# Performance work log

Hardware: AMD Instinct MI355X
Metric: run time of the kernel (lower is better)

Reference implementation:

```python
import jax, jax.numpy as jnp
import numpy as np

B, H, W, C, NH = 16, 56, 56, 192, 6
N = H * W
HD = C // NH
EPS = 1e-5


def _ln(x, g, b):
    m = jnp.mean(x, -1, keepdims=True)
    v = jnp.mean((x - m) ** 2, -1, keepdims=True)
    return (x - m) * jax.lax.rsqrt(v + EPS) * g + b


def _dwconv(x, w, b):
    # x: (B,H,W,Ch), w: (3,3,1,Ch) depthwise, SAME padding
    y = jax.lax.conv_general_dilated(
        x, w, (1, 1), 'SAME',
        dimension_numbers=('NHWC', 'HWIO', 'NHWC'),
        feature_group_count=x.shape[-1])
    return y + b


def _rope_tables():
    k_max = C // 4  # 2D RoPE: feature_dim // (2 * num_spatial_dims)
    theta = 1.0 / (10000.0 ** (jnp.arange(k_max, dtype=jnp.float32) / k_max))
    ai = jnp.arange(H, dtype=jnp.float32)[:, None, None] * theta
    aj = jnp.arange(W, dtype=jnp.float32)[None, :, None] * theta
    ang = jnp.concatenate([jnp.broadcast_to(ai, (H, W, k_max)),
                           jnp.broadcast_to(aj, (H, W, k_max))], -1)  # (H,W,C//2)
    return jnp.cos(ang), jnp.sin(ang)


def _rope(x, cos, sin):
    # x: (B,H,W,C); complex multiply on interleaved (re,im) pairs
    xr, xi = x[..., 0::2], x[..., 1::2]
    return jnp.stack([cos * xr - sin * xi, cos * xi + sin * xr], -1).reshape(x.shape)


def reference(x, cpe1_w, cpe1_b, norm1_g, norm1_b, in_w, in_b, actp_w, actp_b,
              dwc_w, dwc_b, qk_w, qk_b, lepe_w, lepe_b, outp_w, outp_b,
              cpe2_w, cpe2_b, norm2_g, norm2_b, fc1_w, fc1_b, mdw_w, mdw_b,
              fc2_w, fc2_b, mn1_g, mn1_b, mn2_g, mn2_b, mn3_g, mn3_b):
    img = lambda t: t.reshape(B, H, W, -1)
    seq = lambda t: t.reshape(B, N, -1)

    # CPE1
    x = x + seq(_dwconv(img(x), cpe1_w, cpe1_b))
    shortcut = x
    xn = _ln(x, norm1_g, norm1_b)

    # gated branch
    act_res = jax.nn.silu(xn @ actp_w + actp_b)
    h = seq(jax.nn.silu(_dwconv(img(xn @ in_w + in_b), dwc_w, dwc_b)))

    # --- LinearAttention (ELU+1 kernel, RoPE, LePE) ---
    qk = h @ qk_w + qk_b                      # (B,N,2C)
    q = jax.nn.elu(qk[..., :C]) + 1.0
    k = jax.nn.elu(qk[..., C:]) + 1.0
    cos, sin = _rope_tables()
    q_r = seq(_rope(img(q), cos, sin)).reshape(B, N, NH, HD)
    k_r = seq(_rope(img(k), cos, sin)).reshape(B, N, NH, HD)
    q4 = q.reshape(B, N, NH, HD)
    k4 = k.reshape(B, N, NH, HD)
    v4 = h.reshape(B, N, NH, HD)
    kmean = jnp.mean(k4, axis=1)                                  # (B,NH,HD)
    z = 1.0 / (jnp.einsum('bnhd,bhd->bnh', q4, kmean) + 1e-6)     # (B,N,NH)
    kv = jnp.einsum('bnhd,bnhe->bhde', k_r, v4) / N               # (B,NH,HD,HD)
    attn = jnp.einsum('bnhd,bhde->bnhe', q_r, kv) * z[..., None]
    attn = attn.reshape(B, N, C)
    attn = attn + seq(_dwconv(img(h), lepe_w, lepe_b))            # LePE on v

    x = shortcut + (attn * act_res) @ outp_w + outp_b

    # CPE2
    x = x + seq(_dwconv(img(x), cpe2_w, cpe2_b))

    # FRN MLP: fc1 -> dwconv -> 3 chained residual LayerNorms -> GELU -> fc2
    xm = _ln(x, norm2_g, norm2_b)
    f1 = xm @ fc1_w + fc1_b                   # (B,N,768)
    dw = seq(_dwconv(img(f1), mdw_w, mdw_b))
    n1 = _ln(dw + f1, mn1_g, mn1_b)
    n2 = _ln(n1 + f1, mn2_g, mn2_b)
    n3 = _ln(n2 + f1, mn3_g, mn3_b)
    x = x + jax.nn.gelu(n3, approximate=False) @ fc2_w + fc2_b
    return x


def setup_inputs() -> dict:
    key = jax.random.key(0)
    cnt = [0]
    def rn(shape, s=0.05):
        cnt[0] += 1
        return jax.random.normal(jax.random.fold_in(key, cnt[0]), shape, jnp.float32) * s
    dws = (3, 3, 1, C)
    z = lambda n: jnp.zeros((n,), jnp.float32)
    o = lambda n: jnp.ones((n,), jnp.float32)
    return dict(
        x=rn((B, N, C), 1.0),
        cpe1_w=rn(dws), cpe1_b=z(C),
        norm1_g=o(C), norm1_b=z(C),
        in_w=rn((C, C)), in_b=z(C),
        actp_w=rn((C, C)), actp_b=z(C),
        dwc_w=rn(dws), dwc_b=z(C),
        qk_w=rn((C, 2 * C)), qk_b=z(2 * C),
        lepe_w=rn(dws), lepe_b=z(C),
        outp_w=rn((C, C)), outp_b=z(C),
        cpe2_w=rn(dws), cpe2_b=z(C),
        norm2_g=o(C), norm2_b=z(C),
        fc1_w=rn((C, 4 * C)), fc1_b=z(4 * C),
        mdw_w=rn((3, 3, 1, 4 * C)), mdw_b=z(4 * C),
        fc2_w=rn((4 * C, C)), fc2_b=z(C),
        mn1_g=o(4 * C), mn1_b=z(4 * C),
        mn2_g=o(4 * C), mn2_b=z(4 * C),
        mn3_g=o(4 * C), mn3_b=z(4 * C),
    )
```

## Files before the change

kernel.cpp:

```cpp
#include <hip/hip_runtime.h>
#include <hip/hip_bf16.h>
#include <hip/hip_fp16.h>
#include <math.h>

#define BB 16
#define HH 56
#define WW 56
#define CC0 192
#define NHH 6
#define HDD 32
#define NPOS (HH*WW)
#define MROWS (BB*NPOS)
#define C4 (4*CC0)

typedef __hip_bfloat16 bf16;
typedef __half f16;
typedef short short8 __attribute__((ext_vector_type(8)));
typedef short short4v __attribute__((ext_vector_type(4)));
typedef float f32x4 __attribute__((ext_vector_type(4)));
typedef float f32x2 __attribute__((ext_vector_type(2)));
typedef unsigned int u32;
typedef u32 u32x4 __attribute__((ext_vector_type(4)));
typedef u32 u32x2 __attribute__((ext_vector_type(2)));

__device__ __forceinline__ float b2f(bf16 v){ return __bfloat162float(v); }
__device__ __forceinline__ bf16 f2b(float v){ return __float2bfloat16(v); }
__device__ __forceinline__ short f2s(float v){ bf16 b = __float2bfloat16(v); return *(short*)&b; }
__device__ __forceinline__ float s2f(short s){ bf16 b; *(short*)&b = s; return __bfloat162float(b); }
__device__ __forceinline__ float tof(float v){ return v; }
__device__ __forceinline__ float tof(f16 v){ return __half2float(v); }
__device__ __forceinline__ f32x2 bfp(u32 u){
  union { u32 q; float f; } lo, hi;
  lo.q = u << 16; hi.q = u & 0xffff0000u;
  return (f32x2){lo.f, hi.f};
}
__device__ __forceinline__ float fast_gelu(float x){
  float u = 1.5957691216f * (x + 0.044715f*x*x*x);
  float t = 1.f - 2.f/(__expf(u) + 1.f);
  return 0.5f*x*(1.f + t);
}
__device__ __forceinline__ int swz8(int bid, int nblk){
  return (bid & 7) * (nblk >> 3) + (bid >> 3);
}

__global__ __launch_bounds__(256) void convert_weights(
    const float* __restrict__ w0, const float* __restrict__ w1,
    const float* __restrict__ w2, const float* __restrict__ w3,
    const float* __restrict__ w4, const float* __restrict__ w5,
    short* __restrict__ dst){
  int t = blockIdx.x*256 + threadIdx.x;
  int e = t*4;
  if (e >= 479232) return;
  const float* src; int K, N, off;
  if      (e <  36864){ src=w0; K=192; N=192; off=0; }
  else if (e <  73728){ src=w1; K=192; N=192; off=36864; }
  else if (e < 147456){ src=w2; K=192; N=384; off=73728; }
  else if (e < 184320){ src=w3; K=192; N=192; off=147456; }
  else if (e < 331776){ src=w4; K=192; N=768; off=184320; }
  else                { src=w5; K=768; N=192; off=331776; }
  int le = e - off;
  int n = le / K, k = le % K;
  short4v o;
  #pragma unroll
  for (int l = 0; l < 4; ++l) o[l] = f2s(src[(size_t)(k+l)*N + n]);
  *(short4v*)(dst + e) = o;
}

template<typename TIN>
__global__ __launch_bounds__(256) void cpe_ln_kernel(const TIN* __restrict__ in,
    const float* __restrict__ w, const float* __restrict__ bias,
    const float* __restrict__ g, const float* __restrict__ bb,
    f16* __restrict__ x1out, bf16* __restrict__ xnout){
  int wv = threadIdx.x >> 6, lane = threadIdx.x & 63;
  int grp = swz8(blockIdx.x, gridDim.x)*4 + wv;
  int pos0 = grp * 4;
  int b = pos0 / NPOS; int ij = pos0 % NPOS; int i = ij / WW; int j0 = ij % WW;
  int c = lane * 3;
  float acc[4][3];
  {
    float b0 = bias[c], b1 = bias[c+1], b2 = bias[c+2];
    #pragma unroll
    for (int p = 0; p < 4; ++p){ acc[p][0]=b0; acc[p][1]=b1; acc[p][2]=b2; }
  }
  float fc[4][3];
  bool leftOK  = (j0 > 0);
  bool rightOK = (j0 + 4 < WW);
  int base_i = (b*NPOS + i*WW + j0)*CC0 + c;

  #pragma unroll
  for (int di = 0; di < 3; ++di){
    int ii = i + di - 1;
    if (ii < 0 || ii >= HH) continue;
    int rb = base_i + (di-1)*(WW*CC0);
    float wt[3][3];
    #pragma unroll
    for (int dj = 0; dj < 3; ++dj){
      const float* wp = w + (di*3 + dj)*CC0 + c;
      wt[dj][0] = wp[0]; wt[dj][1] = wp[1]; wt[dj][2] = wp[2];
    }
    if (leftOK){
      const TIN* ip = in + rb - CC0;
      float d0 = tof(ip[0]), d1 = tof(ip[1]), d2 = tof(ip[2]);
      acc[0][0] += d0*wt[0][0]; acc[0][1] += d1*wt[0][1]; acc[0][2] += d2*wt[0][2];
    }
    #pragma unroll
    for (int col = 1; col <= 4; ++col){
      const TIN* ip = in + rb + (col-1)*CC0;
      float d0 = tof(ip[0]), d1 = tof(ip[1]), d2 = tof(ip[2]);
      if (di == 1){ fc[col-1][0] = d0; fc[col-1][1] = d1; fc[col-1][2] = d2; }
      #pragma unroll
      for (int dj = 0; dj < 3; ++dj){
        int p = col - dj;
        if (p >= 0 && p < 4){
          acc[p][0] += d0*wt[dj][0]; acc[p][1] += d1*wt[dj][1]; acc[p][2] += d2*wt[dj][2];
        }
      }
    }
    if (rightOK){
      const TIN* ip = in + rb + 4*CC0;
      float d0 = tof(ip[0]), d1 = tof(ip[1]), d2 = tof(ip[2]);
      acc[3][0] += d0*wt[2][0]; acc[3][1] += d1*wt[2][1]; acc[3][2] += d2*wt[2][2];
    }
  }
  float gv0 = g[c], gv1 = g[c+1], gv2 = g[c+2];
  float bv0 = bb[c], bv1 = bb[c+1], bv2 = bb[c+2];
  #pragma unroll
  for (int p = 0; p < 4; ++p){
    float v0 = fc[p][0] + acc[p][0];
    float v1 = fc[p][1] + acc[p][1];
    float v2 = fc[p][2] + acc[p][2];
    int base = (pos0 + p)*CC0 + c;
    f16* xp = x1out + base;
    xp[0] = __float2half(v0); xp[1] = __float2half(v1); xp[2] = __float2half(v2);
    float s = v0+v1+v2, q = v0*v0+v1*v1+v2*v2;
    #pragma unroll
    for (int m = 1; m < 64; m <<= 1){ s += __shfl_xor(s, m, 64); q += __shfl_xor(q, m, 64); }
    float mean = s * (1.f/CC0);
    float rstd = rsqrtf(q * (1.f/CC0) - mean*mean + 1e-5f);
    bf16* op = xnout + base;
    op[0] = f2b((v0-mean)*rstd*gv0 + bv0);
    op[1] = f2b((v1-mean)*rstd*gv1 + bv1);
    op[2] = f2b((v2-mean)*rstd*gv2 + bv2);
  }
}

template<int MODE>
__global__ __launch_bounds__(256) void dwconv4(const bf16* __restrict__ in,
    const float* __restrict__ w, const float* __restrict__ bias, void* __restrict__ out){
  int idx = swz8(blockIdx.x, gridDim.x)*256 + threadIdx.x;
  int cg = idx % 24; int quad = idx / 24;
  int pos0 = quad * 4;
  int b = pos0 / NPOS; int ij = pos0 % NPOS; int i = ij / WW; int j0 = ij % WW;
  int cb = cg * 8;
  const short* fp = (const short*)in;
  f32x2 acc[4][4];
  {
    f32x2 bv0 = *(const f32x2*)(bias + cb);
    f32x2 bv1 = *(const f32x2*)(bias + cb + 2);
    f32x2 bv2 = *(const f32x2*)(bias + cb + 4);
    f32x2 bv3 = *(const f32x2*)(bias + cb + 6);
    #pragma unroll
    for (int p = 0; p < 4; ++p){ acc[p][0]=bv0; acc[p][1]=bv1; acc[p][2]=bv2; acc[p][3]=bv3; }
  }
  bool leftOK  = (j0 > 0);
  bool rightOK = (j0 + 4 < WW);
  int base_i = (b*NPOS + i*WW + j0)*CC0 + cb;

  #pragma unroll
  for (int di = 0; di < 3; ++di){
    int ii = i + di - 1;
    if (ii < 0 || ii >= HH) continue;
    int rb = base_i + (di-1)*(WW*CC0);
    const float* wr = w + (di*3)*CC0 + cb;
    f32x2 wt[3][4];
    #pragma unroll
    for (int dj = 0; dj < 3; ++dj){
      #pragma unroll
      for (int l = 0; l < 4; ++l) wt[dj][l] = *(const f32x2*)(wr + dj*CC0 + 2*l);
    }
    if (leftOK){
      u32x4 x = *(const u32x4*)(fp + rb - CC0);
      #pragma unroll
      for (int l = 0; l < 4; ++l) acc[0][l] += bfp(x[l])*wt[0][l];
    }
    #pragma unroll
    for (int col = 1; col <= 4; ++col){
      u32x4 x = *(const u32x4*)(fp + rb + (col-1)*CC0);
      f32x2 dv[4];
      #pragma unroll
      for (int l = 0; l < 4; ++l) dv[l] = bfp(x[l]);
      #pragma unroll
      for (int dj = 0; dj < 3; ++dj){
        int p = col - dj;
        if (p >= 0 && p < 4){
          #pragma unroll
          for (int l = 0; l < 4; ++l) acc[p][l] += dv[l]*wt[dj][l];
        }
      }
    }
    if (rightOK){
      u32x4 x = *(const u32x4*)(fp + rb + 4*CC0);
      #pragma unroll
      for (int l = 0; l < 4; ++l) acc[3][l] += bfp(x[l])*wt[2][l];
    }
  }
  #pragma unroll
  for (int p = 0; p < 4; ++p){
    int oidx = (pos0 + p)*CC0 + cb;
    short8 o;
    if constexpr (MODE == 1){
      #pragma unroll
      for (int l = 0; l < 4; ++l){
        float a0 = acc[p][l][0], a1 = acc[p][l][1];
        o[2*l]   = f2s(a0/(1.f + expf(-a0)));
        o[2*l+1] = f2s(a1/(1.f + expf(-a1)));
      }
    } else {
      u32x4 r = *(const u32x4*)((const short*)out + oidx);
      #pragma unroll
      for (int l = 0; l < 4; ++l){
        f32x2 s = bfp(r[l]) + acc[p][l];
        o[2*l] = f2s(s[0]); o[2*l+1] = f2s(s[1]);
      }
    }
    *(short8*)((short*)out + oidx) = o;
  }
}

#define BM 256
#define BN 64
#define BK 32
#define LDA 40
template<int K, int N, int ALOAD, int EPI>
__global__ __launch_bounds__(256) void mfma_gemm(
    const void* __restrict__ a0v, const void* __restrict__ a1v,
    const short* __restrict__ wT, const float* __restrict__ bias,
    const void* __restrict__ addf, void* __restrict__ out0, void* __restrict__ out1){
  __shared__ short As[BM*LDA];
  __shared__ short Bs[BN*LDA];
  int tid = threadIdx.x;
  int wave = tid >> 6, lane = tid & 63;
  size_t m0 = (size_t)blockIdx.x * BM;
  int n0 = blockIdx.y * BN;
  int wm = wave * 64;
  int am = lane & 15, ak = (lane >> 4) * 8;

  f32x4 acc[4][4];
  #pragma unroll
  for (int mt = 0; mt < 4; ++mt)
    #pragma unroll
    for (int nt = 0; nt < 4; ++nt)
      acc[mt][nt] = (f32x4){0.f,0.f,0.f,0.f};

  for (int k0 = 0; k0 < K; k0 += BK){
    if constexpr (ALOAD == 0){
      const short* A = (const short*)a0v;
      #pragma unroll
      for (int it = 0; it < 4; ++it){
        int idx = it*256 + tid;
        int row = idx >> 2; int ko = (idx & 3) * 8;
        short8 v = *(const short8*)(A + (m0 + row)*(size_t)K + k0 + ko);
        *(short8*)&As[row*LDA + ko] = v;
      }
    } else {
      const short* A0p = (const short*)a0v;
      const short* A1p = (const short*)a1v;
      #pragma unroll
      for (int it = 0; it < 4; ++it){
        int idx = it*256 + tid;
        int row = idx >> 2; int ko = (idx & 3) * 8;
        size_t off = (m0 + row)*(size_t)K + k0 + ko;
        short8 va = *(const short8*)(A0p + off);
        short8 vb = *(const short8*)(A1p + off);
        short8 o;
        #pragma unroll
        for (int l = 0; l < 8; ++l) o[l] = f2s(s2f(va[l]) * s2f(vb[l]));
        *(short8*)&As[row*LDA + ko] = o;
      }
    }
    {
      int row = tid >> 2; int ko = (tid & 3) * 8;
      short8 v = *(const short8*)(wT + (size_t)(n0 + row)*K + k0 + ko);
      *(short8*)&Bs[row*LDA + ko] = v;
    }
    __syncthreads();
    short8 af[4], bfr[4];
    #pragma unroll
    for (int mt = 0; mt < 4; ++mt) af[mt] = *(short8*)&As[(wm + mt*16 + am)*LDA + ak];
    #pragma unroll
    for (int nt = 0; nt < 4; ++nt) bfr[nt] = *(short8*)&Bs[(nt*16 + am)*LDA + ak];
    #pragma unroll
    for (int mt = 0; mt < 4; ++mt)
      #pragma unroll
      for (int nt = 0; nt < 4; ++nt)
        acc[mt][nt] = __builtin_amdgcn_mfma_f32_16x16x32_bf16(af[mt], bfr[nt], acc[mt][nt], 0, 0, 0);
    __syncthreads();
  }

  int cn = lane & 15;
  int cr = (lane >> 4) * 4;
  #pragma unroll
  for (int mt = 0; mt < 4; ++mt){
    #pragma unroll
    for (int nt = 0; nt < 4; ++nt){
      int gn = n0 + nt*16 + cn;
      float bv;
      if constexpr (EPI == 4) bv = (n0 < CC0) ? bias[gn] : ((const float*)addf)[gn - CC0];
      else bv = bias[gn];
      #pragma unroll
      for (int r = 0; r < 4; ++r){
        size_t gm = m0 + wm + mt*16 + cr + r;
        float v = acc[mt][nt][r] + bv;
        if constexpr (EPI == 0){
          ((bf16*)out0)[gm*N + gn] = f2b(v);
        } else if constexpr (EPI == 1){
          ((bf16*)out0)[gm*N + gn] = f2b(v / (1.f + expf(-v)));
        } else if constexpr (EPI == 2){
          float rv = (v > 0.f) ? (v + 1.f) : expf(v);
          if (n0 < CC0) ((bf16*)out0)[gm*CC0 + gn] = f2b(rv);
          else          ((bf16*)out1)[gm*CC0 + (gn - CC0)] = f2b(rv);
        } else if constexpr (EPI == 4){
          if (n0 < CC0) ((bf16*)out0)[gm*CC0 + gn] = f2b(v / (1.f + expf(-v)));
          else          ((bf16*)out1)[gm*CC0 + (gn - CC0)] = f2b(v);
        } else if constexpr (EPI == 5){
          ((f16*)out0)[gm*N + gn] =
            __float2half(__half2float(((const f16*)addf)[gm*N + gn]) + v);
        } else {
          ((float*)out0)[gm*N + gn] =
            __half2float(((const f16*)addf)[gm*N + gn]) + v;
        }
      }
    }
  }
}

__global__ void rope_tables_kernel(float* __restrict__ cosT, float* __restrict__ sinT){
  int idx = blockIdx.x*256 + threadIdx.x;
  if (idx >= NPOS*96) return;
  int t = idx % 96; int ij = idx / 96; int i = ij / WW; int j = ij % WW;
  int kk = (t < 48) ? t : (t - 48);
  float th = expf(-(float)kk * 0.19188209108283716f);
  float pos = (t < 48) ? (float)i : (float)j;
  float ang = pos * th;
  cosT[idx] = cosf(ang);
  sinT[idx] = sinf(ang);
}

#define KVCH 14
__global__ __launch_bounds__(256) void kv_kernel(const bf16* __restrict__ kbuf,
    const bf16* __restrict__ hbuf, const float* __restrict__ cosT,
    const float* __restrict__ sinT, float* __restrict__ kv,
    float* __restrict__ kmean){
  int bi = blockIdx.x;
  int chunk = bi % KVCH; bi /= KVCH;
  int h = bi % NHH; int b = bi / NHH;
  int tid = threadIdx.x;
  int r8 = tid >> 5, lane = tid & 31;
  __shared__ float krs[8][32];
  __shared__ float vvs[8][32];
  int d = tid >> 3; int ebase = (tid & 7) * 4;
  float a0 = 0.f, a1 = 0.f, a2 = 0.f, a3 = 0.f;
  float ksum = 0.f;
  int c = h*HDD + lane;
  int t = c >> 1;
  bool odd = (lane & 1);
  for (int step = 0; step < NPOS/(KVCH*8); ++step){
    int n = chunk*(NPOS/KVCH) + step*8 + r8;
    size_t row = (size_t)b*NPOS + n;
    float kc = b2f(kbuf[row*CC0 + c]);
    float kp = b2f(kbuf[row*CC0 + (c ^ 1)]);
    ksum += kc;
    float cs = cosT[(size_t)n*96 + t], sn = sinT[(size_t)n*96 + t];
    krs[r8][lane] = odd ? (cs*kc + sn*kp) : (cs*kc - sn*kp);
    vvs[r8][lane] = b2f(hbuf[row*CC0 + c]);
    __syncthreads();
    #pragma unroll
    for (int nn = 0; nn < 8; ++nn){
      float kk2 = krs[nn][d];
      a0 += kk2 * vvs[nn][ebase+0];
      a1 += kk2 * vvs[nn][ebase+1];
      a2 += kk2 * vvs[nn][ebase+2];
      a3 += kk2 * vvs[nn][ebase+3];
    }
    __syncthreads();
  }
  const float invN = 1.f/NPOS;
  ksum += __shfl_xor(ksum, 32, 64);
  if ((tid & 32) == 0) atomicAdd(&kmean[b*CC0 + c], ksum * invN);
  float* kvp = kv + (((size_t)(b*NHH + h)*HDD + d)*HDD) + ebase;
  atomicAdd(kvp+0, a0*invN);
  atomicAdd(kvp+1, a1*invN);
  atomicAdd(kvp+2, a2*invN);
  atomicAdd(kvp+3, a3*invN);
}

__global__ __launch_bounds__(256) void attn_mfma(const bf16* __restrict__ q,
    const float* __restrict__ kmean, const float* __restrict__ kv,
    const float* __restrict__ cosT, const float* __restrict__ sinT,
    bf16* __restrict__ out){
  int w = threadIdx.x >> 6, lane = threadIdx.x & 63;
  int idx = blockIdx.x*4 + w;
  int mt = idx % (NPOS/16);
  int rest = idx / (NPOS/16);
  int h = rest % NHH; int b = rest / NHH;
  int r15 = lane & 15, kq = (lane >> 4) * 8;
  int n = mt*16 + r15;
  size_t row = (size_t)b*NPOS + n;
  int ch = h*HDD + kq;
  short8 q8 = *(const short8*)((const short*)q + row*CC0 + ch);
  float qf[8];
  #pragma unroll
  for (int j = 0; j < 8; ++j) qf[j] = s2f(q8[j]);
  const float* kmp = kmean + b*CC0 + ch;
  f32x4 km0 = *(const f32x4*)(kmp);
  f32x4 km1 = *(const f32x4*)(kmp + 4);
  float pm = qf[0]*km0[0]+qf[1]*km0[1]+qf[2]*km0[2]+qf[3]*km0[3]
           + qf[4]*km1[0]+qf[5]*km1[1]+qf[6]*km1[2]+qf[7]*km1[3];
  pm += __shfl_xor(pm, 16, 64);
  pm += __shfl_xor(pm, 32, 64);
  float z = 1.f/(pm + 1e-6f);
  int t0 = h*16 + (kq >> 1);
  f32x4 cs = *(const f32x4*)(cosT + n*96 + t0);
  f32x4 sn = *(const f32x4*)(sinT + n*96 + t0);
  short8 af;
  #pragma unroll
  for (int u = 0; u < 4; ++u){
    float e = cs[u]*qf[2*u]   - sn[u]*qf[2*u+1];
    float o = cs[u]*qf[2*u+1] + sn[u]*qf[2*u];
    af[2*u] = f2s(e); af[2*u+1] = f2s(o);
  }
  const float* kvp = kv + (size_t)(b*NHH + h)*HDD*HDD + kq*HDD + r15;
  short8 bf0, bf1;
  #pragma unroll
  for (int j = 0; j < 8; ++j){
    bf0[j] = f2s(kvp[j*HDD]);
    bf1[j] = f2s(kvp[j*HDD + 16]);
  }
  f32x4 acc0 = (f32x4){0.f,0.f,0.f,0.f};
  f32x4 acc1 = (f32x4){0.f,0.f,0.f,0.f};
  acc0 = __builtin_amdgcn_mfma_f32_16x16x32_bf16(af, bf0, acc0, 0, 0, 0);
  acc1 = __builtin_amdgcn_mfma_f32_16x16x32_bf16(af, bf1, acc1, 0, 0, 0);
  int rbase = (lane >> 4) * 4;
  #pragma unroll
  for (int r = 0; r < 4; ++r){
    float zz = __shfl(z, rbase + r, 64);
    size_t orow = (size_t)b*NPOS + mt*16 + rbase + r;
    out[orow*CC0 + ch - kq + r15]      = f2b(acc0[r]*zz);
    out[orow*CC0 + ch - kq + r15 + 16] = f2b(acc1[r]*zz);
  }
}

__global__ __launch_bounds__(256) void mdw_ln_kernel(const bf16* __restrict__ f1,
    const float* __restrict__ w, const float* __restrict__ bias,
    const float* __restrict__ g1, const float* __restrict__ b1,
    const float* __restrict__ g2, const float* __restrict__ b2,
    const float* __restrict__ g3, const float* __restrict__ b3,
    bf16* __restrict__ out){
  int wv = threadIdx.x >> 6, lane = threadIdx.x & 63;
  int grp = swz8(blockIdx.x, gridDim.x)*4 + wv;
  int pos0 = grp * 4;
  int b = pos0 / NPOS; int ij = pos0 % NPOS; int i = ij / WW; int j0 = ij % WW;
  int c0 = lane * 8;
  int c1 = 512 + lane * 4;
  const short* fp = (const short*)f1;

  f32x2 acc2[4][6];
  {
    f32x2 bv[6];
    #pragma unroll
    for (int l = 0; l < 4; ++l) bv[l] = *(const f32x2*)(bias + c0 + 2*l);
    bv[4] = *(const f32x2*)(bias + c1);
    bv[5] = *(const f32x2*)(bias + c1 + 2);
    #pragma unroll
    for (int p = 0; p < 4; ++p)
      #pragma unroll
      for (int l = 0; l < 6; ++l) acc2[p][l] = bv[l];
  }
  u32x4 fca[4]; u32x2 fcb[4];
  bool leftOK  = (j0 > 0);
  bool rightOK = (j0 + 4 < WW);
  int base_i = (b*NPOS + i*WW + j0)*C4;

  #pragma unroll
  for (int di = 0; di < 3; ++di){
    int ii = i + di - 1;
    if (ii < 0 || ii >= HH) continue;
    int rb = base_i + (di-1)*(WW*C4);
    f32x2 wt2[3][6];
    #pragma unroll
    for (int dj = 0; dj < 3; ++dj){
      const float* wp = w + (di*3 + dj)*C4;
      #pragma unroll
      for (int l = 0; l < 4; ++l) wt2[dj][l] = *(const f32x2*)(wp + c0 + 2*l);
      wt2[dj][4] = *(const f32x2*)(wp + c1);
      wt2[dj][5] = *(const f32x2*)(wp + c1 + 2);
    }
    if (leftOK){
      u32x4 xa = *(const u32x4*)(fp + rb - C4 + c0);
      u32x2 xb = *(const u32x2*)(fp + rb - C4 + c1);
      f32x2 dv[6];
      dv[0]=bfp(xa[0]); dv[1]=bfp(xa[1]); dv[2]=bfp(xa[2]); dv[3]=bfp(xa[3]);
      dv[4]=bfp(xb[0]); dv[5]=bfp(xb[1]);
      #pragma unroll
      for (int l = 0; l < 6; ++l) acc2[0][l] += dv[l]*wt2[0][l];
    }
    #pragma unroll
    for (int col = 1; col <= 4; ++col){
      int off = rb + (col-1)*C4;
      u32x4 xa = *(const u32x4*)(fp + off + c0);
      u32x2 xb = *(const u32x2*)(fp + off + c1);
      if (di == 1){ fca[col-1] = xa; fcb[col-1] = xb; }
      f32x2 dv[6];
      dv[0]=bfp(xa[0]); dv[1]=bfp(xa[1]); dv[2]=bfp(xa[2]); dv[3]=bfp(xa[3]);
      dv[4]=bfp(xb[0]); dv[5]=bfp(xb[1]);
      #pragma unroll
      for (int dj = 0; dj < 3; ++dj){
        int p = col - dj;
        if (p >= 0 && p < 4){
          #pragma unroll
          for (int l = 0; l < 6; ++l) acc2[p][l] += dv[l]*wt2[dj][l];
        }
      }
    }
    if (rightOK){
      u32x4 xa = *(const u32x4*)(fp + rb + 4*C4 + c0);
      u32x2 xb = *(const u32x2*)(fp + rb + 4*C4 + c1);
      f32x2 dv[6];
      dv[0]=bfp(xa[0]); dv[1]=bfp(xa[1]); dv[2]=bfp(xa[2]); dv[3]=bfp(xa[3]);
      dv[4]=bfp(xb[0]); dv[5]=bfp(xb[1]);
      #pragma unroll
      for (int l = 0; l < 6; ++l) acc2[3][l] += dv[l]*wt2[2][l];
    }
  }
  #pragma unroll
  for (int p = 0; p < 4; ++p){
    #pragma unroll
    for (int l = 0; l < 4; ++l) acc2[p][l] += bfp(fca[p][l]);
    acc2[p][4] += bfp(fcb[p][0]);
    acc2[p][5] += bfp(fcb[p][1]);
  }

  const float* gs[3] = {g1, g2, g3};
  const float* bs[3] = {b1, b2, b3};
  #pragma unroll
  for (int pass = 0; pass < 3; ++pass){
    f32x2 gv[6], bvv[6];
    #pragma unroll
    for (int l = 0; l < 4; ++l){
      gv[l]  = *(const f32x2*)(gs[pass] + c0 + 2*l);
      bvv[l] = *(const f32x2*)(bs[pass] + c0 + 2*l);
    }
    gv[4]  = *(const f32x2*)(gs[pass] + c1);  gv[5]  = *(const f32x2*)(gs[pass] + c1 + 2);
    bvv[4] = *(const f32x2*)(bs[pass] + c1);  bvv[5] = *(const f32x2*)(bs[pass] + c1 + 2);
    #pragma unroll
    for (int p = 0; p < 4; ++p){
      f32x2 s2 = acc2[p][0];
      f32x2 q2 = acc2[p][0]*acc2[p][0];
      #pragma unroll
      for (int l = 1; l < 6; ++l){ s2 += acc2[p][l]; q2 += acc2[p][l]*acc2[p][l]; }
      float s = s2[0]+s2[1], q = q2[0]+q2[1];
      #pragma unroll
      for (int m = 1; m < 64; m <<= 1){ s += __shfl_xor(s, m, 64); q += __shfl_xor(q, m, 64); }
      float mean = s * (1.f/C4);
      float rstd = rsqrtf(q * (1.f/C4) - mean*mean + 1e-5f);
      #pragma unroll
      for (int l = 0; l < 6; ++l){
        f32x2 rg = gv[l]*rstd;
        f32x2 t  = acc2[p][l] - mean;
        acc2[p][l] = t*rg + bvv[l];
      }
      if (pass < 2){
        #pragma unroll
        for (int l = 0; l < 4; ++l) acc2[p][l] += bfp(fca[p][l]);
        acc2[p][4] += bfp(fcb[p][0]);
        acc2[p][5] += bfp(fcb[p][1]);
      }
    }
  }
  #pragma unroll
  for (int p = 0; p < 4; ++p){
    short8 o0; short4v o1;
    #pragma unroll
    for (int l = 0; l < 4; ++l){
      o0[2*l]   = f2s(fast_gelu(acc2[p][l][0]));
      o0[2*l+1] = f2s(fast_gelu(acc2[p][l][1]));
    }
    o1[0] = f2s(fast_gelu(acc2[p][4][0]));
    o1[1] = f2s(fast_gelu(acc2[p][4][1]));
    o1[2] = f2s(fast_gelu(acc2[p][5][0]));
    o1[3] = f2s(fast_gelu(acc2[p][5][1]));
    int ob = (pos0 + p)*C4;
    *(short8*)((short*)out + ob + c0) = o0;
    *(short4v*)((short*)out + ob + c1) = o1;
  }
}

extern "C" void kernel_launch(void* const* d_in, const int* in_sizes, int n_in,
                              void* d_out, int out_size, void* d_ws, size_t ws_size,
                              hipStream_t stream){
  (void)in_sizes; (void)n_in; (void)out_size; (void)ws_size;
  const float* X      = (const float*)d_in[0];
  const float* cpe1_w = (const float*)d_in[1];
  const float* cpe1_b = (const float*)d_in[2];
  const float* n1g    = (const float*)d_in[3];
  const float* n1b    = (const float*)d_in[4];
  const float* in_w   = (const float*)d_in[5];
  const float* in_b   = (const float*)d_in[6];
  const float* actp_w = (const float*)d_in[7];
  const float* actp_b = (const float*)d_in[8];
  const float* dwc_w  = (const float*)d_in[9];
  const float* dwc_b  = (const float*)d_in[10];
  const float* qk_w   = (const float*)d_in[11];
  const float* qk_b   = (const float*)d_in[12];
  const float* lepe_w = (const float*)d_in[13];
  const float* lepe_b = (const float*)d_in[14];
  const float* outp_w = (const float*)d_in[15];
  const float* outp_b = (const float*)d_in[16];
  const float* cpe2_w = (const float*)d_in[17];
  const float* cpe2_b = (const float*)d_in[18];
  const float* n2g    = (const float*)d_in[19];
  const float* n2b    = (const float*)d_in[20];
  const float* fc1_w  = (const float*)d_in[21];
  const float* fc1_b  = (const float*)d_in[22];
  const float* mdw_w  = (const float*)d_in[23];
  const float* mdw_b  = (const float*)d_in[24];
  const float* fc2_w  = (const float*)d_in[25];
  const float* fc2_b  = (const float*)d_in[26];
  const float* mn1g   = (const float*)d_in[27];
  const float* mn1b   = (const float*)d_in[28];
  const float* mn2g   = (const float*)d_in[29];
  const float* mn2b   = (const float*)d_in[30];
  const float* mn3g   = (const float*)d_in[31];
  const float* mn3b   = (const float*)d_in[32];

  char* ws = (char*)d_ws;
  const size_t SZF = (size_t)MROWS*CC0*4;
  const size_t SZB = (size_t)MROWS*CC0*2;
  f16* A0h = (f16*)(ws);
  char* base2 = ws + SZF;
  bf16* BQ = (bf16*)(base2 + 0*SZB);
  bf16* BKb= (bf16*)(base2 + 1*SZB);
  bf16* BA = (bf16*)(base2 + 2*SZB);
  bf16* B1 = (bf16*)(base2 + 3*SZB);
  bf16* B0 = (bf16*)(base2 + 4*SZB);
  bf16* B2 = (bf16*)(base2 + 5*SZB);
  bf16* B3 = (bf16*)(base2 + 6*SZB);
  f16*  A1h = (f16*)(base2);
  bf16*  F1 = (bf16*)(base2);
  bf16*  DW = (bf16*)(base2 + 4*SZB);
  short* WT = (short*)(base2 + 8*SZB);
  char* tail = (char*)(WT + 479232 + 64);
  float* KMEAN = (float*)tail;                 tail += (size_t)BB*CC0*4;
  float* KV    = (float*)tail;                 tail += (size_t)BB*NHH*HDD*HDD*4;
  float* COS   = (float*)tail;                 tail += (size_t)NPOS*96*4;
  float* SIN   = (float*)tail;

  const short* actpT = WT + 0;
  const short* qkT   = WT + 73728;
  const short* outpT = WT + 147456;
  const short* fc1T  = WT + 184320;
  const short* fc2T  = WT + 331776;

  const int GPOS16 = MROWS/16;
  const int GDW4   = (MROWS/4)*24/256;
  const int GATT   = (BB*NHH*(NPOS/16))/4;

  convert_weights<<<(479232/4 + 255)/256, 256, 0, stream>>>(actp_w, in_w, qk_w, outp_w, fc1_w, fc2_w, WT);
  rope_tables_kernel<<<(NPOS*96 + 255)/256, 256, 0, stream>>>(COS, SIN);
  cpe_ln_kernel<float><<<GPOS16, 256, 0, stream>>>(X, cpe1_w, cpe1_b, n1g, n1b, A0h, B0);
  mfma_gemm<CC0,2*CC0,0,4><<<dim3(MROWS/BM,2*CC0/BN), 256, 0, stream>>>(B0, nullptr, actpT, actp_b, in_b, B1, B2);
  dwconv4<1><<<GDW4, 256, 0, stream>>>(B2, dwc_w, dwc_b, B3);
  mfma_gemm<CC0,2*CC0,0,2><<<dim3(MROWS/BM,2*CC0/BN), 256, 0, stream>>>(B3, nullptr, qkT, qk_b, nullptr, BQ, BKb);
  hipMemsetAsync(KMEAN, 0, (size_t)BB*CC0*4, stream);
  hipMemsetAsync(KV, 0, (size_t)BB*NHH*HDD*HDD*4, stream);
  kv_kernel<<<BB*NHH*KVCH, 256, 0, stream>>>(BKb, B3, COS, SIN, KV, KMEAN);
  attn_mfma<<<GATT, 256, 0, stream>>>(BQ, KMEAN, KV, COS, SIN, BA);
  dwconv4<2><<<GDW4, 256, 0, stream>>>(B3, lepe_w, lepe_b, BA);
  mfma_gemm<CC0,CC0,1,5><<<dim3(MROWS/BM,CC0/BN), 256, 0, stream>>>(BA, B1, outpT, outp_b, A0h, A1h, nullptr);
  cpe_ln_kernel<f16><<<GPOS16, 256, 0, stream>>>(A1h, cpe2_w, cpe2_b, n2g, n2b, A0h, B0);
  mfma_gemm<CC0,C4,0,0><<<dim3(MROWS/BM,C4/BN), 256, 0, stream>>>(B0, nullptr, fc1T, fc1_b, nullptr, F1, nullptr);
  mdw_ln_kernel<<<GPOS16, 256, 0, stream>>>(F1, mdw_w, mdw_b, mn1g, mn1b, mn2g, mn2b, mn3g, mn3b, DW);
  mfma_gemm<C4,CC0,0,3><<<dim3(MROWS/BM,CC0/BN), 256, 0, stream>>>(DW, nullptr, fc2T, fc2_b, A0h, d_out, nullptr);
}
```

Before: 562.2 us.

## Merge setup kernels, reorder GEMM grid, widen fc1 tile, batch mdw loads

Folds weight conversion, RoPE table generation and the KMEAN/KV zeroing into a single setup kernel, which removes two launches and two memsets. The GEMM grid is swapped so blockIdx.x walks N tiles, letting neighbouring blocks share the same A rows in cache. The fc1 GEMM now uses a 128-wide N tile, so each loaded A tile is reused across more columns, at the cost of more accumulator registers. The mdw conv now issues all six column loads before its FMAs to raise memory-level parallelism, which also raises register pressure.

```diff
diff --git a/kernel.cpp b/kernel.cpp
--- a/kernel.cpp
+++ b/kernel.cpp
@@ -43,27 +43,41 @@
   return (bid & 7) * (nblk >> 3) + (bid >> 3);
 }
 
-__global__ __launch_bounds__(256) void convert_weights(
+__global__ __launch_bounds__(256) void setup_kernel(
     const float* __restrict__ w0, const float* __restrict__ w1,
     const float* __restrict__ w2, const float* __restrict__ w3,
     const float* __restrict__ w4, const float* __restrict__ w5,
-    short* __restrict__ dst){
-  int t = blockIdx.x*256 + threadIdx.x;
-  int e = t*4;
-  if (e >= 479232) return;
-  const float* src; int K, N, off;
-  if      (e <  36864){ src=w0; K=192; N=192; off=0; }
-  else if (e <  73728){ src=w1; K=192; N=192; off=36864; }
-  else if (e < 147456){ src=w2; K=192; N=384; off=73728; }
-  else if (e < 184320){ src=w3; K=192; N=192; off=147456; }
-  else if (e < 331776){ src=w4; K=192; N=768; off=184320; }
-  else                { src=w5; K=768; N=192; off=331776; }
-  int le = e - off;
-  int n = le / K, k = le % K;
-  short4v o;
-  #pragma unroll
-  for (int l = 0; l < 4; ++l) o[l] = f2s(src[(size_t)(k+l)*N + n]);
-  *(short4v*)(dst + e) = o;
+    short* __restrict__ dst, float* __restrict__ cosT, float* __restrict__ sinT,
+    float* __restrict__ zbase){
+  int bid = blockIdx.x;
+  if (bid < 468){
+    int e = (bid*256 + threadIdx.x)*4;
+    const float* src; int K, N, off;
+    if      (e <  36864){ src=w0; K=192; N=192; off=0; }
+    else if (e <  73728){ src=w1; K=192; N=192; off=36864; }
+    else if (e < 147456){ src=w2; K=192; N=384; off=73728; }
+    else if (e < 184320){ src=w3; K=192; N=192; off=147456; }
+    else if (e < 331776){ src=w4; K=192; N=768; off=184320; }
+    else                { src=w5; K=768; N=192; off=331776; }
+    int le = e - off;
+    int n = le / K, k = le % K;
+    short4v o;
+    #pragma unroll
+    for (int l = 0; l < 4; ++l) o[l] = f2s(src[(size_t)(k+l)*N + n]);
+    *(short4v*)(dst + e) = o;
+  } else if (bid < 468 + 1176){
+    int idx = (bid-468)*256 + threadIdx.x;
+    int t = idx % 96; int ij = idx / 96; int i = ij / WW; int j = ij % WW;
+    int kk = (t < 48) ? t : (t - 48);
+    float th = expf(-(float)kk * 0.19188209108283716f);
+    float pos = (t < 48) ? (float)i : (float)j;
+    float ang = pos * th;
+    cosT[idx] = cosf(ang);
+    sinT[idx] = sinf(ang);
+  } else {
+    int zi = ((bid-1644)*256 + threadIdx.x)*4;
+    if (zi < 101376) *(f32x4*)(zbase + zi) = (f32x4){0.f,0.f,0.f,0.f};
+  }
 }
 
 template<typename TIN>
@@ -228,28 +242,28 @@
 }
 
 #define BM 256
-#define BN 64
 #define BK 32
 #define LDA 40
-template<int K, int N, int ALOAD, int EPI>
+template<int K, int N, int NB, int ALOAD, int EPI>
 __global__ __launch_bounds__(256) void mfma_gemm(
     const void* __restrict__ a0v, const void* __restrict__ a1v,
     const short* __restrict__ wT, const float* __restrict__ bias,
     const void* __restrict__ addf, void* __restrict__ out0, void* __restrict__ out1){
   __shared__ short As[BM*LDA];
-  __shared__ short Bs[BN*LDA];
+  __shared__ short Bs[NB*LDA];
+  constexpr int NT = NB/16;
   int tid = threadIdx.x;
   int wave = tid >> 6, lane = tid & 63;
-  size_t m0 = (size_t)blockIdx.x * BM;
-  int n0 = blockIdx.y * BN;
+  size_t m0 = (size_t)blockIdx.y * BM;
+  int n0 = blockIdx.x * NB;
   int wm = wave * 64;
   int am = lane & 15, ak = (lane >> 4) * 8;
 
-  f32x4 acc[4][4];
+  f32x4 acc[4][NT];
   #pragma unroll
   for (int mt = 0; mt < 4; ++mt)
     #pragma unroll
-    for (int nt = 0; nt < 4; ++nt)
+    for (int nt = 0; nt < NT; ++nt)
       acc[mt][nt] = (f32x4){0.f,0.f,0.f,0.f};
 
   for (int k0 = 0; k0 < K; k0 += BK){
@@ -278,21 +292,23 @@
         *(short8*)&As[row*LDA + ko] = o;
       }
     }
-    {
-      int row = tid >> 2; int ko = (tid & 3) * 8;
+    #pragma unroll
+    for (int bt = 0; bt < NB/64; ++bt){
+      int idx2 = bt*256 + tid;
+      int row = idx2 >> 2; int ko = (idx2 & 3) * 8;
       short8 v = *(const short8*)(wT + (size_t)(n0 + row)*K + k0 + ko);
       *(short8*)&Bs[row*LDA + ko] = v;
     }
     __syncthreads();
-    short8 af[4], bfr[4];
+    short8 af[4], bfr[NT];
     #pragma unroll
     for (int mt = 0; mt < 4; ++mt) af[mt] = *(short8*)&As[(wm + mt*16 + am)*LDA + ak];
     #pragma unroll
-    for (int nt = 0; nt < 4; ++nt) bfr[nt] = *(short8*)&Bs[(nt*16 + am)*LDA + ak];
+    for (int nt = 0; nt < NT; ++nt) bfr[nt] = *(short8*)&Bs[(nt*16 + am)*LDA + ak];
     #pragma unroll
     for (int mt = 0; mt < 4; ++mt)
       #pragma unroll
-      for (int nt = 0; nt < 4; ++nt)
+      for (int nt = 0; nt < NT; ++nt)
         acc[mt][nt] = __builtin_amdgcn_mfma_f32_16x16x32_bf16(af[mt], bfr[nt], acc[mt][nt], 0, 0, 0);
     __syncthreads();
   }
@@ -302,7 +318,7 @@
   #pragma unroll
   for (int mt = 0; mt < 4; ++mt){
     #pragma unroll
-    for (int nt = 0; nt < 4; ++nt){
+    for (int nt = 0; nt < NT; ++nt){
       int gn = n0 + nt*16 + cn;
       float bv;
       if constexpr (EPI == 4) bv = (n0 < CC0) ? bias[gn] : ((const float*)addf)[gn - CC0];
@@ -332,18 +348,6 @@
       }
     }
   }
-}
-
-__global__ void rope_tables_kernel(float* __restrict__ cosT, float* __restrict__ sinT){
-  int idx = blockIdx.x*256 + threadIdx.x;
-  if (idx >= NPOS*96) return;
-  int t = idx % 96; int ij = idx / 96; int i = ij / WW; int j = ij % WW;
-  int kk = (t < 48) ? t : (t - 48);
-  float th = expf(-(float)kk * 0.19188209108283716f);
-  float pos = (t < 48) ? (float)i : (float)j;
-  float ang = pos * th;
-  cosT[idx] = cosf(ang);
-  sinT[idx] = sinf(ang);
 }
 
 #define KVCH 14
@@ -486,6 +490,18 @@
     int ii = i + di - 1;
     if (ii < 0 || ii >= HH) continue;
     int rb = base_i + (di-1)*(WW*C4);
+    u32x4 xa6[6]; u32x2 xb6[6];
+    if (leftOK){ xa6[0] = *(const u32x4*)(fp + rb - C4 + c0);
+                 xb6[0] = *(const u32x2*)(fp + rb - C4 + c1); }
+    else       { xa6[0] = (u32x4){0,0,0,0}; xb6[0] = (u32x2){0,0}; }
+    #pragma unroll
+    for (int col = 1; col <= 4; ++col){
+      xa6[col] = *(const u32x4*)(fp + rb + (col-1)*C4 + c0);
+      xb6[col] = *(const u32x2*)(fp + rb + (col-1)*C4 + c1);
+    }
+    if (rightOK){ xa6[5] = *(const u32x4*)(fp + rb + 4*C4 + c0);
+                  xb6[5] = *(const u32x2*)(fp + rb + 4*C4 + c1); }
+    else        { xa6[5] = (u32x4){0,0,0,0}; xb6[5] = (u32x2){0,0}; }
     f32x2 wt2[3][6];
     #pragma unroll
     for (int dj = 0; dj < 3; ++dj){
@@ -495,24 +511,13 @@
       wt2[dj][4] = *(const f32x2*)(wp + c1);
       wt2[dj][5] = *(const f32x2*)(wp + c1 + 2);
     }
-    if (leftOK){
-      u32x4 xa = *(const u32x4*)(fp + rb - C4 + c0);
-      u32x2 xb = *(const u32x2*)(fp + rb - C4 + c1);
+    #pragma unroll
+    for (int col = 0; col < 6; ++col){
+      if (di == 1 && col >= 1 && col <= 4){ fca[col-1] = xa6[col]; fcb[col-1] = xb6[col]; }
       f32x2 dv[6];
-      dv[0]=bfp(xa[0]); dv[1]=bfp(xa[1]); dv[2]=bfp(xa[2]); dv[3]=bfp(xa[3]);
-      dv[4]=bfp(xb[0]); dv[5]=bfp(xb[1]);
-      #pragma unroll
-      for (int l = 0; l < 6; ++l) acc2[0][l] += dv[l]*wt2[0][l];
-    }
-    #pragma unroll
-    for (int col = 1; col <= 4; ++col){
-      int off = rb + (col-1)*C4;
-      u32x4 xa = *(const u32x4*)(fp + off + c0);
-      u32x2 xb = *(const u32x2*)(fp + off + c1);
-      if (di == 1){ fca[col-1] = xa; fcb[col-1] = xb; }
-      f32x2 dv[6];
-      dv[0]=bfp(xa[0]); dv[1]=bfp(xa[1]); dv[2]=bfp(xa[2]); dv[3]=bfp(xa[3]);
-      dv[4]=bfp(xb[0]); dv[5]=bfp(xb[1]);
+      dv[0]=bfp(xa6[col][0]); dv[1]=bfp(xa6[col][1]);
+      dv[2]=bfp(xa6[col][2]); dv[3]=bfp(xa6[col][3]);
+      dv[4]=bfp(xb6[col][0]); dv[5]=bfp(xb6[col][1]);
       #pragma unroll
       for (int dj = 0; dj < 3; ++dj){
         int p = col - dj;
@@ -521,15 +526,6 @@
           for (int l = 0; l < 6; ++l) acc2[p][l] += dv[l]*wt2[dj][l];
         }
       }
-    }
-    if (rightOK){
-      u32x4 xa = *(const u32x4*)(fp + rb + 4*C4 + c0);
-      u32x2 xb = *(const u32x2*)(fp + rb + 4*C4 + c1);
-      f32x2 dv[6];
-      dv[0]=bfp(xa[0]); dv[1]=bfp(xa[1]); dv[2]=bfp(xa[2]); dv[3]=bfp(xa[3]);
-      dv[4]=bfp(xb[0]); dv[5]=bfp(xb[1]);
-      #pragma unroll
-      for (int l = 0; l < 6; ++l) acc2[3][l] += dv[l]*wt2[2][l];
     }
   }
   #pragma unroll
@@ -665,20 +661,18 @@
   const int GDW4   = (MROWS/4)*24/256;
   const int GATT   = (BB*NHH*(NPOS/16))/4;
 
-  convert_weights<<<(479232/4 + 255)/256, 256, 0, stream>>>(actp_w, in_w, qk_w, outp_w, fc1_w, fc2_w, WT);
-  rope_tables_kernel<<<(NPOS*96 + 255)/256, 256, 0, stream>>>(COS, SIN);
+  setup_kernel<<<1743, 256, 0, stream>>>(actp_w, in_w, qk_w, outp_w, fc1_w, fc2_w,
+                                         WT, COS, SIN, KMEAN);
   cpe_ln_kernel<float><<<GPOS16, 256, 0, stream>>>(X, cpe1_w, cpe1_b, n1g, n1b, A0h, B0);
-  mfma_gemm<CC0,2*CC0,0,4><<<dim3(MROWS/BM,2*CC0/BN), 256, 0, stream>>>(B0, nullptr, actpT, actp_b, in_b, B1, B2);
+  mfma_gemm<CC0,2*CC0,64,0,4><<<dim3(2*CC0/64,MROWS/BM), 256, 0, stream>>>(B0, nullptr, actpT, actp_b, in_b, B1, B2);
   dwconv4<1><<<GDW4, 256, 0, stream>>>(B2, dwc_w, dwc_b, B3);
-  mfma_gemm<CC0,2*CC0,0,2><<<dim3(MROWS/BM,2*CC0/BN), 256, 0, stream>>>(B3, nullptr, qkT, qk_b, nullptr, BQ, BKb);
-  hipMemsetAsync(KMEAN, 0, (size_t)BB*CC0*4, stream);
-  hipMemsetAsync(KV, 0, (size_t)BB*NHH*HDD*HDD*4, stream);
+  mfma_gemm<CC0,2*CC0,64,0,2><<<dim3(2*CC0/64,MROWS/BM), 256, 0, stream>>>(B3, nullptr, qkT, qk_b, nullptr, BQ, BKb);
   kv_kernel<<<BB*NHH*KVCH, 256, 0, stream>>>(BKb, B3, COS, SIN, KV, KMEAN);
   attn_mfma<<<GATT, 256, 0, stream>>>(BQ, KMEAN, KV, COS, SIN, BA);
   dwconv4<2><<<GDW4, 256, 0, stream>>>(B3, lepe_w, lepe_b, BA);
-  mfma_gemm<CC0,CC0,1,5><<<dim3(MROWS/BM,CC0/BN), 256, 0, stream>>>(BA, B1, outpT, outp_b, A0h, A1h, nullptr);
+  mfma_gemm<CC0,CC0,64,1,5><<<dim3(CC0/64,MROWS/BM), 256, 0, stream>>>(BA, B1, outpT, outp_b, A0h, A1h, nullptr);
   cpe_ln_kernel<f16><<<GPOS16, 256, 0, stream>>>(A1h, cpe2_w, cpe2_b, n2g, n2b, A0h, B0);
-  mfma_gemm<CC0,C4,0,0><<<dim3(MROWS/BM,C4/BN), 256, 0, stream>>>(B0, nullptr, fc1T, fc1_b, nullptr, F1, nullptr);
+  mfma_gemm<CC0,C4,128,0,0><<<dim3(C4/128,MROWS/BM), 256, 0, stream>>>(B0, nullptr, fc1T, fc1_b, nullptr, F1, nullptr);
   mdw_ln_kernel<<<GPOS16, 256, 0, stream>>>(F1, mdw_w, mdw_b, mn1g, mn1b, mn2g, mn2b, mn3g, mn3b, DW);
-  mfma_gemm<C4,CC0,0,3><<<dim3(MROWS/BM,CC0/BN), 256, 0, stream>>>(DW, nullptr, fc2T, fc2_b, A0h, d_out, nullptr);
-}
+  mfma_gemm<C4,CC0,64,0,3><<<dim3(CC0/64,MROWS/BM), 256, 0, stream>>>(DW, nullptr, fc2T, fc2_b, A0h, d_out, nullptr);
+}
```

Measured after the change: 576.9 us. 2.6% more time.
